# Performance work log

Measured on AMD Instinct MI355X. Metric: run time of the kernel, lower is better.

Reference implementation:

```python
import jax, jax.numpy as jnp
import numpy as np

IN_DIM = 128
HIDDEN_DIM = 128
N_NODES = 100000
N_EDGES = 1000000


def setup_inputs() -> dict:
    key = jax.random.key(0)
    k_z, k_e, k_w1, k_b1, k_w2, k_b2 = jax.random.split(key, 6)
    z = jax.random.normal(k_z, (N_NODES, IN_DIM), dtype=jnp.float32)
    edge_index = jax.random.randint(k_e, (2, N_EDGES), 0, N_NODES, dtype=jnp.int64)
    # torch Linear init: U(-1/sqrt(fan_in), 1/sqrt(fan_in))
    lim1 = 1.0 / np.sqrt(2 * IN_DIM)
    W1 = jax.random.uniform(k_w1, (2 * IN_DIM, HIDDEN_DIM), minval=-lim1, maxval=lim1, dtype=jnp.float32)
    b1 = jax.random.uniform(k_b1, (HIDDEN_DIM,), minval=-lim1, maxval=lim1, dtype=jnp.float32)
    lim2 = 1.0 / np.sqrt(HIDDEN_DIM)
    W2 = jax.random.uniform(k_w2, (HIDDEN_DIM, 1), minval=-lim2, maxval=lim2, dtype=jnp.float32)
    b2 = jax.random.uniform(k_b2, (1,), minval=-lim2, maxval=lim2, dtype=jnp.float32)
    return {"z": z, "edge_index": edge_index, "W1": W1, "b1": b1, "W2": W2, "b2": b2}


def reference(z, edge_index, W1, b1, W2, b2):
    src, dst = edge_index[0], edge_index[1]
    h = jnp.concatenate([z[src], z[dst]], axis=1)      # [E, 2*in_dim]
    h = jax.nn.relu(h @ W1 + b1)                        # [E, hidden]
    return jax.nn.sigmoid(h @ W2 + b2).reshape(-1)      # [E]
```

## Files before the change

### kernel.cpp

```cpp
#include <hip/hip_runtime.h>
#include <hip/hip_fp16.h>
#include <math.h>

#define IN_DIM 128
#define HID    128
#define NN     100000
#define WPACK_BYTES (64 * 64 * 16)
#define WPACK_OFF   64
#define UBF_OFF     (WPACK_OFF + WPACK_BYTES + 192)
#define UBF_BYTES   (NN * HID)
#define VBF_OFF     (UBF_OFF + UBF_BYTES)
#define VBF_BYTES   (NN * HID)

typedef __attribute__((ext_vector_type(8))) __bf16 bf16x8;
typedef __attribute__((ext_vector_type(4))) float  f32x4;
typedef __attribute__((ext_vector_type(2))) float  f32x2;

__device__ __forceinline__ unsigned pk2bf(float a, float b) {
    union { __bf16 h[2]; unsigned u; } r;
    r.h[0] = (__bf16)a; r.h[1] = (__bf16)b;
    return r.u;
}
__device__ __forceinline__ bf16x8 asbf(uint4 v) { return __builtin_bit_cast(bf16x8, v); }

__global__ void prep(const float* __restrict__ W1,
                     const unsigned* __restrict__ ei,
                     uint4* __restrict__ wpack,
                     int* __restrict__ flag, int do_pack) {
    const int t = threadIdx.x;
    if (t < 64) {
        unsigned v = ei[2 * t + 1];
        unsigned long long b = __ballot(v != 0u);
        if (t == 0) flag[0] = (b == 0ull) ? 1 : 0;
    }
    if (!do_pack) return;
    const int lane = t & 63;
    #pragma unroll
    for (int fi = 0; fi < 16; ++fi) {
        const int frag = (t >> 6) + fi * 4;
        const int kc = frag >> 3, jsg = frag & 7;
        const int k0 = kc * 32 + (lane >> 4) * 8;
        const int j  = jsg * 16 + (lane & 15);
        unsigned wv[4];
        #pragma unroll
        for (int p = 0; p < 4; ++p)
            wv[p] = pk2bf(W1[(k0 + 2 * p) * HID + j], W1[(k0 + 2 * p + 1) * HID + j]);
        wpack[frag * 64 + lane] = make_uint4(wv[0], wv[1], wv[2], wv[3]);
    }
}

__global__ __launch_bounds__(256)
void uv_gemm(const float* __restrict__ z,
             const uint4* __restrict__ wpack,
             char* __restrict__ ubf, char* __restrict__ vbf,
             int nwt)
{
    const int t = threadIdx.x, lane = t & 63, w = t >> 6;
    const int l4 = lane & 15, q = lane >> 4;
    const int jh = w & 1;
    char* obuf = (w >= 2) ? vbf : ubf;

    uint4 Bf[4][4];
    #pragma unroll
    for (int kc = 0; kc < 4; ++kc)
        #pragma unroll
        for (int jsg = 0; jsg < 4; ++jsg)
            Bf[kc][jsg] = wpack[((((w >> 1) * 4 + kc) * 8) + jh * 4 + jsg) * 64 + lane];

    for (int wt = blockIdx.x; wt < nwt; wt += gridDim.x) {
        #pragma unroll
        for (int kc = 0; kc < 4; ++kc)
            #pragma unroll
            for (int jsg = 0; jsg < 4; ++jsg)
                asm volatile("" : "+v"(Bf[kc][jsg].x), "+v"(Bf[kc][jsg].y),
                                  "+v"(Bf[kc][jsg].z), "+v"(Bf[kc][jsg].w));

        const int node0 = wt * 16;
        const float* zr = z + (long long)(node0 + l4) * IN_DIM + q * 8;

        f32x4 acc[4] = {};
        #pragma unroll
        for (int kc = 0; kc < 4; ++kc) {
            const float4 f0 = *reinterpret_cast<const float4*>(zr + kc * 32);
            const float4 f1 = *reinterpret_cast<const float4*>(zr + kc * 32 + 4);
            const bf16x8 a = asbf(make_uint4(pk2bf(f0.x, f0.y), pk2bf(f0.z, f0.w),
                                             pk2bf(f1.x, f1.y), pk2bf(f1.z, f1.w)));
            #pragma unroll
            for (int jsg = 0; jsg < 4; ++jsg)
                acc[jsg] = __builtin_amdgcn_mfma_f32_16x16x32_bf16(
                    a, asbf(Bf[kc][jsg]), acc[jsg], 0, 0, 0);
        }

        #pragma unroll
        for (int reg = 0; reg < 4; ++reg) {
            const int n = node0 + q * 4 + reg;
            int pk = __builtin_amdgcn_cvt_pk_fp8_f32(acc[0][reg], acc[1][reg], 0, false);
            pk = __builtin_amdgcn_cvt_pk_fp8_f32(acc[2][reg], acc[3][reg], pk, true);
            *reinterpret_cast<int*>(obuf + (long long)n * 128 + jh * 64 + l4 * 4) = pk;
        }
    }
}

__global__ __launch_bounds__(256)
void lp_edge(const char* __restrict__ ubf, const char* __restrict__ vbf,
             const int* __restrict__ ei32,
             const float* __restrict__ b1, const float* __restrict__ W2,
             const float* __restrict__ b2, float* __restrict__ out,
             const int* __restrict__ flag, int E)
{
    const int t = threadIdx.x;
    const int g = t & 15;
    const int use64 = flag[0];
    const int jh = g >> 3, la = 2 * (g & 7), lb = la + 1;

    f32x2 b1f[4], w2f[4];
    #pragma unroll
    for (int p = 0; p < 2; ++p) {
        const int l = p ? lb : la;
        b1f[2 * p]     = f32x2{b1[jh * 64 + l],      b1[jh * 64 + 16 + l]};
        b1f[2 * p + 1] = f32x2{b1[jh * 64 + 32 + l], b1[jh * 64 + 48 + l]};
        w2f[2 * p]     = f32x2{W2[jh * 64 + l],      W2[jh * 64 + 16 + l]};
        w2f[2 * p + 1] = f32x2{W2[jh * 64 + 32 + l], W2[jh * 64 + 48 + l]};
    }
    const f32x2 zf2 = {0.f, 0.f};
    const float b2v = b2[0];

#define EDOT(ACC, UU, VV)                                                     \
    {                                                                         \
        f32x2 q0 = __builtin_amdgcn_cvt_pk_f32_fp8(UU.x, false)               \
                 + __builtin_amdgcn_cvt_pk_f32_fp8(VV.x, false) + b1f[0];     \
        f32x2 q1 = __builtin_amdgcn_cvt_pk_f32_fp8(UU.x, true)                \
                 + __builtin_amdgcn_cvt_pk_f32_fp8(VV.x, true) + b1f[1];      \
        f32x2 q2 = __builtin_amdgcn_cvt_pk_f32_fp8(UU.y, false)               \
                 + __builtin_amdgcn_cvt_pk_f32_fp8(VV.y, false) + b1f[2];     \
        f32x2 q3 = __builtin_amdgcn_cvt_pk_f32_fp8(UU.y, true)                \
                 + __builtin_amdgcn_cvt_pk_f32_fp8(VV.y, true) + b1f[3];      \
        q0 = __builtin_elementwise_max(q0, zf2);                              \
        q1 = __builtin_elementwise_max(q1, zf2);                              \
        q2 = __builtin_elementwise_max(q2, zf2);                              \
        q3 = __builtin_elementwise_max(q3, zf2);                              \
        ACC = fmaf(q0.x, w2f[0].x, fmaf(q0.y, w2f[0].y, ACC));                \
        ACC = fmaf(q1.x, w2f[1].x, fmaf(q1.y, w2f[1].y, ACC));                \
        ACC = fmaf(q2.x, w2f[2].x, fmaf(q2.y, w2f[2].y, ACC));                \
        ACC = fmaf(q3.x, w2f[3].x, fmaf(q3.y, w2f[3].y, ACC));                \
    }

    for (int e2 = blockIdx.x * 32 + ((t >> 4) << 1); e2 < E; e2 += gridDim.x * 32) {
        const int e3 = min(e2 + 1, E - 1);
        int s0 = ei32[(long long)e2 << use64];
        int d0 = ei32[(long long)(E + e2) << use64];
        int s1 = ei32[(long long)e3 << use64];
        int d1 = ei32[(long long)(E + e3) << use64];
        s0 = min(max(s0, 0), NN - 1); d0 = min(max(d0, 0), NN - 1);
        s1 = min(max(s1, 0), NN - 1); d1 = min(max(d1, 0), NN - 1);
        const uint2 uu0 = *reinterpret_cast<const uint2*>(ubf + (long long)s0 * 128 + g * 8);
        const uint2 vv0 = *reinterpret_cast<const uint2*>(vbf + (long long)d0 * 128 + g * 8);
        const uint2 uu1 = *reinterpret_cast<const uint2*>(ubf + (long long)s1 * 128 + g * 8);
        const uint2 vv1 = *reinterpret_cast<const uint2*>(vbf + (long long)d1 * 128 + g * 8);

        float sum0 = 0.f, sum1 = 0.f;
        EDOT(sum0, uu0, vv0)
        EDOT(sum1, uu1, vv1)

        #pragma unroll
        for (int o = 1; o <= 8; o <<= 1) {
            sum0 += __shfl_xor(sum0, o);
            sum1 += __shfl_xor(sum1, o);
        }
        if (g < 2) {
            const int e = e2 + g;
            if (e < E && (g == 0 || e3 == e2 + 1))
                out[e] = 1.f / (1.f + expf(-((g ? sum1 : sum0) + b2v)));
        }
    }
#undef EDOT
}

__global__ __launch_bounds__(256, 3)
void lp_main(const float* __restrict__ z,
             const int* __restrict__ ei32,
             const float* __restrict__ W1,
             const float* __restrict__ b1,
             const float* __restrict__ W2,
             const float* __restrict__ b2,
             float* __restrict__ out,
             const int* __restrict__ flag,
             const uint4* __restrict__ wpack,
             int use_ws, int E, int ntiles)
{
    __shared__ uint4 ldsA_[64 * 512 / 16];
    __shared__ float part[4][64];
    char* ldsc = (char*)ldsA_;

    const int t = threadIdx.x, lane = t & 63, w = t >> 6;
    const int use64 = flag[0];

    uint4 Bf[8][2];
    if (use_ws) {
        #pragma unroll
        for (int kc = 0; kc < 8; ++kc)
            #pragma unroll
            for (int js = 0; js < 2; ++js)
                Bf[kc][js] = wpack[(kc * 8 + (w * 2 + js)) * 64 + lane];
    } else {
        #pragma unroll
        for (int kc = 0; kc < 8; ++kc)
            #pragma unroll
            for (int js = 0; js < 2; ++js) {
                const int k0 = kc * 32 + (lane >> 4) * 8;
                const int j  = (w * 2 + js) * 16 + (lane & 15);
                unsigned wv[4];
                #pragma unroll
                for (int p = 0; p < 4; ++p)
                    wv[p] = pk2bf(W1[(k0 + 2 * p) * HID + j],
                                  W1[(k0 + 2 * p + 1) * HID + j]);
                Bf[kc][js] = make_uint4(wv[0], wv[1], wv[2], wv[3]);
            }
    }

    const int e_r = lane & 15, q = lane >> 4, m16 = q * 16;
    const float b1v0 = b1[w * 32 + e_r], b1v1 = b1[w * 32 + 16 + e_r];
    const float w2v0 = W2[w * 32 + e_r], w2v1 = W2[w * 32 + 16 + e_r];
    const float b2v  = b2[0];

    for (int tile = blockIdx.x; tile < ntiles; tile += gridDim.x) {
        const int e0 = tile * 64;
        #pragma unroll 8
        for (int i = 0; i < 16; ++i) {
            const int el = i * 4 + w;
            int e = e0 + el; if (e > E - 1) e = E - 1;
            const int word = (lane < 32) ? e : (E + e);
            int node = ei32[(long long)word << use64];
            node = min(max(node, 0), NN - 1);
            const float4 v = *reinterpret_cast<const float4*>(
                &z[node * IN_DIM + (lane & 31) * 4]);
            const int byte = el * 512 + ((lane * 8) ^ ((el & 7) << 4));
            *reinterpret_cast<uint2*>(ldsc + byte) =
                make_uint2(pk2bf(v.x, v.y), pk2bf(v.z, v.w));
        }
        __syncthreads();

        f32x4 acc[4][2] = {};
        #pragma unroll
        for (int kc = 0; kc < 8; ++kc) {
            #pragma unroll
            for (int es = 0; es < 4; ++es) {
                const int row  = es * 16 + e_r;
                const int byte = row * 512 + ((kc * 64 + m16) ^ ((row & 7) << 4));
                const bf16x8 a = *reinterpret_cast<const bf16x8*>(ldsc + byte);
                acc[es][0] = __builtin_amdgcn_mfma_f32_16x16x32_bf16(
                    a, asbf(Bf[kc][0]), acc[es][0], 0, 0, 0);
                acc[es][1] = __builtin_amdgcn_mfma_f32_16x16x32_bf16(
                    a, asbf(Bf[kc][1]), acc[es][1], 0, 0, 0);
            }
        }

        float v16[16];
        #pragma unroll
        for (int es = 0; es < 4; ++es)
            #pragma unroll
            for (int reg = 0; reg < 4; ++reg)
                v16[es * 4 + reg] = fmaxf(acc[es][0][reg] + b1v0, 0.f) * w2v0
                                  + fmaxf(acc[es][1][reg] + b1v1, 0.f) * w2v1;
        #pragma unroll
        for (int rnd = 0; rnd < 4; ++rnd) {
            const int o = 1 << rnd, hl = 8 >> rnd;
            #pragma unroll
            for (int i = 0; i < hl; ++i) {
                const float a = v16[i], b = v16[i + hl];
                const float s = (lane & o) ? a : b;
                const float r = __shfl_xor(s, o);
                v16[i] = ((lane & o) ? b : a) + r;
            }
        }
        {
            const int lx  = lane & 15;
            const int idx = ((lx & 1) << 3) | ((lx & 2) << 1) | ((lx & 4) >> 1) | ((lx & 8) >> 3);
            const int edge = (idx >> 2) * 16 + q * 4 + (idx & 3);
            part[w][edge] = v16[0];
        }
        __syncthreads();

        if (t < 64) {
            const int e = e0 + t;
            if (e < E) {
                const float s = part[0][t] + part[1][t] + part[2][t] + part[3][t] + b2v;
                out[e] = 1.f / (1.f + expf(-s));
            }
        }
    }
}

extern "C" void kernel_launch(void* const* d_in, const int* in_sizes, int n_in,
                              void* d_out, int out_size, void* d_ws, size_t ws_size,
                              hipStream_t stream) {
    const float* z  = (const float*)d_in[0];
    const void*  ei = d_in[1];
    const float* W1 = (const float*)d_in[2];
    const float* b1 = (const float*)d_in[3];
    const float* W2 = (const float*)d_in[4];
    const float* b2 = (const float*)d_in[5];
    float* out = (float*)d_out;
    int*   flag  = (int*)d_ws;
    uint4* wpack = (uint4*)((char*)d_ws + WPACK_OFF);
    char*  ubf   = (char*)d_ws + UBF_OFF;
    char*  vbf   = (char*)d_ws + VBF_OFF;

    const int E = in_sizes[1] / 2;
    const int use_ws = (ws_size >= (size_t)(WPACK_OFF + WPACK_BYTES)) ? 1 : 0;
    const int use_uv = (ws_size >= (size_t)(VBF_OFF + VBF_BYTES)) ? 1 : 0;

    hipLaunchKernelGGL(prep, dim3(1), dim3(256), 0, stream,
                       W1, (const unsigned*)ei, wpack, flag, use_ws);

    if (use_uv) {
        const int nwt = NN / 16;
        hipLaunchKernelGGL(uv_gemm, dim3(1024), dim3(256), 0, stream,
                           z, wpack, ubf, vbf, nwt);
        hipLaunchKernelGGL(lp_edge, dim3(2048), dim3(256), 0, stream,
                           ubf, vbf, (const int*)ei, b1, W2, b2, out, flag, E);
    } else {
        const int ntiles = (E + 63) / 64;
        const int grid = (ntiles < 768) ? ntiles : 768;
        hipLaunchKernelGGL(lp_main, dim3(grid), dim3(256), 0, stream,
                           z, (const int*)ei, W1, b1, W2, b2, out, flag, wpack,
                           use_ws, E, ntiles);
    }
}
```

Measured before the change: 82.36 us.

## Parallelize weight packing and restructure node GEMM with LDS-staged weights

Result: faster. 80.27 us (-2.5%).

```diff
diff --git a/kernel.cpp b/kernel.cpp
--- a/kernel.cpp
+++ b/kernel.cpp
@@ -28,25 +28,22 @@
                      uint4* __restrict__ wpack,
                      int* __restrict__ flag, int do_pack) {
     const int t = threadIdx.x;
-    if (t < 64) {
+    if (blockIdx.x == 0 && t < 64) {
         unsigned v = ei[2 * t + 1];
         unsigned long long b = __ballot(v != 0u);
         if (t == 0) flag[0] = (b == 0ull) ? 1 : 0;
     }
     if (!do_pack) return;
     const int lane = t & 63;
-    #pragma unroll
-    for (int fi = 0; fi < 16; ++fi) {
-        const int frag = (t >> 6) + fi * 4;
-        const int kc = frag >> 3, jsg = frag & 7;
-        const int k0 = kc * 32 + (lane >> 4) * 8;
-        const int j  = jsg * 16 + (lane & 15);
-        unsigned wv[4];
-        #pragma unroll
-        for (int p = 0; p < 4; ++p)
-            wv[p] = pk2bf(W1[(k0 + 2 * p) * HID + j], W1[(k0 + 2 * p + 1) * HID + j]);
-        wpack[frag * 64 + lane] = make_uint4(wv[0], wv[1], wv[2], wv[3]);
-    }
+    const int frag = (t >> 6) + blockIdx.x * 4;
+    const int kc = frag >> 3, jsg = frag & 7;
+    const int k0 = kc * 32 + (lane >> 4) * 8;
+    const int j  = jsg * 16 + (lane & 15);
+    unsigned wv[4];
+    #pragma unroll
+    for (int p = 0; p < 4; ++p)
+        wv[p] = pk2bf(W1[(k0 + 2 * p) * HID + j], W1[(k0 + 2 * p + 1) * HID + j]);
+    wpack[frag * 64 + lane] = make_uint4(wv[0], wv[1], wv[2], wv[3]);
 }
 
 __global__ __launch_bounds__(256)
@@ -55,49 +52,50 @@
              char* __restrict__ ubf, char* __restrict__ vbf,
              int nwt)
 {
+    __shared__ uint4 Wlds[16 * 64];
     const int t = threadIdx.x, lane = t & 63, w = t >> 6;
     const int l4 = lane & 15, q = lane >> 4;
-    const int jh = w & 1;
-    char* obuf = (w >= 2) ? vbf : ubf;
-
-    uint4 Bf[4][4];
-    #pragma unroll
-    for (int kc = 0; kc < 4; ++kc)
-        #pragma unroll
-        for (int jsg = 0; jsg < 4; ++jsg)
-            Bf[kc][jsg] = wpack[((((w >> 1) * 4 + kc) * 8) + jh * 4 + jsg) * 64 + lane];
-
-    for (int wt = blockIdx.x; wt < nwt; wt += gridDim.x) {
-        #pragma unroll
-        for (int kc = 0; kc < 4; ++kc)
-            #pragma unroll
-            for (int jsg = 0; jsg < 4; ++jsg)
-                asm volatile("" : "+v"(Bf[kc][jsg].x), "+v"(Bf[kc][jsg].y),
-                                  "+v"(Bf[kc][jsg].z), "+v"(Bf[kc][jsg].w));
-
-        const int node0 = wt * 16;
-        const float* zr = z + (long long)(node0 + l4) * IN_DIM + q * 8;
-
-        f32x4 acc[4] = {};
-        #pragma unroll
-        for (int kc = 0; kc < 4; ++kc) {
-            const float4 f0 = *reinterpret_cast<const float4*>(zr + kc * 32);
-            const float4 f1 = *reinterpret_cast<const float4*>(zr + kc * 32 + 4);
-            const bf16x8 a = asbf(make_uint4(pk2bf(f0.x, f0.y), pk2bf(f0.z, f0.w),
-                                             pk2bf(f1.x, f1.y), pk2bf(f1.z, f1.w)));
-            #pragma unroll
-            for (int jsg = 0; jsg < 4; ++jsg)
-                acc[jsg] = __builtin_amdgcn_mfma_f32_16x16x32_bf16(
-                    a, asbf(Bf[kc][jsg]), acc[jsg], 0, 0, 0);
-        }
-
-        #pragma unroll
-        for (int reg = 0; reg < 4; ++reg) {
-            const int n = node0 + q * 4 + reg;
-            int pk = __builtin_amdgcn_cvt_pk_fp8_f32(acc[0][reg], acc[1][reg], 0, false);
-            pk = __builtin_amdgcn_cvt_pk_fp8_f32(acc[2][reg], acc[3][reg], pk, true);
-            *reinterpret_cast<int*>(obuf + (long long)n * 128 + jh * 64 + l4 * 4) = pk;
-        }
+    const int tg = blockIdx.x >> 2;
+    const int qd = blockIdx.x & 3;
+    const int uv = qd >> 1, jh = qd & 1;
+    char* obuf = uv ? vbf : ubf;
+
+    #pragma unroll
+    for (int i = 0; i < 4; ++i) {
+        const int idx = i * 256 + t;
+        const int fi = idx >> 6, ln = idx & 63;
+        const int kc = fi >> 2, jsg = fi & 3;
+        Wlds[fi * 64 + ln] =
+            wpack[(((uv * 4 + kc) * 8) + jh * 4 + jsg) * 64 + ln];
+    }
+    __syncthreads();
+
+    const int wt = tg * 4 + w;
+    if (wt >= nwt) return;
+    const int node0 = wt * 16;
+    const float* zr = z + (long long)(node0 + l4) * IN_DIM + q * 8;
+
+    f32x4 acc[4] = {};
+    #pragma unroll
+    for (int kc = 0; kc < 4; ++kc) {
+        const float4 f0 = *reinterpret_cast<const float4*>(zr + kc * 32);
+        const float4 f1 = *reinterpret_cast<const float4*>(zr + kc * 32 + 4);
+        const bf16x8 a = asbf(make_uint4(pk2bf(f0.x, f0.y), pk2bf(f0.z, f0.w),
+                                         pk2bf(f1.x, f1.y), pk2bf(f1.z, f1.w)));
+        #pragma unroll
+        for (int jsg = 0; jsg < 4; ++jsg) {
+            const uint4 b = Wlds[(kc * 4 + jsg) * 64 + lane];
+            acc[jsg] = __builtin_amdgcn_mfma_f32_16x16x32_bf16(
+                a, asbf(b), acc[jsg], 0, 0, 0);
+        }
+    }
+
+    #pragma unroll
+    for (int reg = 0; reg < 4; ++reg) {
+        const int n = node0 + q * 4 + reg;
+        int pk = __builtin_amdgcn_cvt_pk_fp8_f32(acc[0][reg], acc[1][reg], 0, false);
+        pk = __builtin_amdgcn_cvt_pk_fp8_f32(acc[2][reg], acc[3][reg], pk, true);
+        *reinterpret_cast<int*>(obuf + (long long)n * 128 + jh * 64 + l4 * 4) = pk;
     }
 }
 
@@ -310,12 +308,13 @@
     const int use_ws = (ws_size >= (size_t)(WPACK_OFF + WPACK_BYTES)) ? 1 : 0;
     const int use_uv = (ws_size >= (size_t)(VBF_OFF + VBF_BYTES)) ? 1 : 0;
 
-    hipLaunchKernelGGL(prep, dim3(1), dim3(256), 0, stream,
+    hipLaunchKernelGGL(prep, dim3(16), dim3(256), 0, stream,
                        W1, (const unsigned*)ei, wpack, flag, use_ws);
 
     if (use_uv) {
         const int nwt = NN / 16;
-        hipLaunchKernelGGL(uv_gemm, dim3(1024), dim3(256), 0, stream,
+        const int ngrp = (nwt + 3) / 4;
+        hipLaunchKernelGGL(uv_gemm, dim3(ngrp * 4), dim3(256), 0, stream,
                            z, wpack, ubf, vbf, nwt);
         hipLaunchKernelGGL(lp_edge, dim3(2048), dim3(256), 0, stream,
                            ubf, vbf, (const int*)ei, b1, W2, b2, out, flag, E);
```
